# Kernel tuning notes

Measured on AMD Instinct MI355X. Metric: run time of the kernel, lower is better.

## Reference

```python
import jax, jax.numpy as jnp
import numpy as np

# Gemma3-style config (matches init_kwargs)
NUM_HEADS = 8
NUM_KV_GROUPS = 4
HEAD_DIM = 256
GROUP_SIZE = NUM_HEADS // NUM_KV_GROUPS
SLIDING_WINDOW = 1024
QUERY_PRE_ATTN_SCALAR = 256.0
SCALE = QUERY_PRE_ATTN_SCALAR ** (-0.5)
EPS = 1e-6


def rmsnorm(x, scale):
    # Gemma-style RMSNorm: fp32 variance, zero-centered weight with (1 + scale)
    xf = x.astype(jnp.float32)
    var = jnp.mean(xf * xf, axis=-1, keepdims=True)
    out = xf * jax.lax.rsqrt(var + EPS) * (1.0 + scale.astype(jnp.float32))
    return out.astype(x.dtype)


def sliding_causal_mask(q_len, kv_len, dtype):
    # additive mask [q_len, kv_len]: 0 allowed, -inf blocked
    q_pos = jnp.arange(kv_len - q_len, kv_len)[:, None]
    k_pos = jnp.arange(kv_len)[None, :]
    allowed = (k_pos <= q_pos) & (k_pos >= q_pos - SLIDING_WINDOW + 1)
    return jnp.where(allowed, jnp.zeros((), dtype), jnp.array(-jnp.inf, dtype))


def setup_inputs() -> dict:
    key = jax.random.key(0)
    ks = jax.random.split(key, 5)
    B, T, D = 2, 2048, 2560
    H, G, Hd = NUM_HEADS, NUM_KV_GROUPS, HEAD_DIM
    x = jax.random.normal(ks[0], (B, T, D), dtype=jnp.float32)
    Wq = jax.random.normal(ks[1], (D, H * Hd), dtype=jnp.float32) * 0.02
    Wk = jax.random.normal(ks[2], (D, G * Hd), dtype=jnp.float32) * 0.02
    Wv = jax.random.normal(ks[3], (D, G * Hd), dtype=jnp.float32) * 0.02
    Wo = jax.random.normal(ks[4], (H * Hd, D), dtype=jnp.float32) * 0.02
    q_scale = jnp.zeros((Hd,), dtype=jnp.float32)
    k_scale = jnp.zeros((Hd,), dtype=jnp.float32)
    return {"x": x, "Wq": Wq, "Wk": Wk, "Wv": Wv, "Wo": Wo,
            "q_scale": q_scale, "k_scale": k_scale}


def reference(x, Wq, Wk, Wv, Wo, q_scale, k_scale):
    B, T, D = x.shape
    H, G, g, Hd = NUM_HEADS, NUM_KV_GROUPS, GROUP_SIZE, HEAD_DIM
    # projections
    q = (x @ Wq).reshape(B, T, H, Hd).transpose(0, 2, 1, 3)   # [B,H,T,Hd]
    k = (x @ Wk).reshape(B, T, G, Hd).transpose(0, 2, 1, 3)   # [B,G,T,Hd]
    v = (x @ Wv).reshape(B, T, G, Hd).transpose(0, 2, 1, 3)   # [B,G,T,Hd]
    # qk-norm
    q = rmsnorm(q, q_scale)
    k = rmsnorm(k, k_scale)
    S = T  # no past_kv (prefill)
    # faithful reproduction of the module's head-group reshapes
    q = q.reshape(B, G, g, T, Hd).reshape(B * g, G, T, Hd)
    k = jnp.broadcast_to(k[:, None], (B, g, G, S, Hd)).reshape(B * g, G, S, Hd)
    v = jnp.broadcast_to(v[:, None], (B, g, G, S, Hd)).reshape(B * g, G, S, Hd)
    mask = sliding_causal_mask(T, S, q.dtype)  # [T,S]
    scores = jnp.einsum('bgtd,bgsd->bgts', q, k) * SCALE + mask
    attn = jax.nn.softmax(scores, axis=-1)
    out = jnp.einsum('bgts,bgsd->bgtd', attn, v)
    # faithful inverse reshapes (note g/G order swap vs input, as in source)
    out = out.reshape(B, g, G, T, Hd).reshape(B, H, T, Hd)
    out = out.transpose(0, 2, 1, 3).reshape(B, T, H * Hd)
    return out @ Wo
```

## Files before the change

### kernel.cpp

```cpp
#include <hip/hip_runtime.h>
#include <hip/hip_bf16.h>

typedef unsigned short u16;

#define T_SEQ 2048
#define NTOK 4096
#define D_MODEL 2560
#define NQKV 4096
#define WIN 1024
#define ATTN_SCALE 0.0625f
#define SMAX 17.0f
#define KROW 264

typedef __attribute__((ext_vector_type(8))) short bf16x8;
typedef __attribute__((ext_vector_type(8))) unsigned short u16x8;
typedef __attribute__((ext_vector_type(4))) float f32x4;

__device__ __forceinline__ float bf2f(u16 u) {
  union { unsigned int i; float f; } c; c.i = ((unsigned int)u) << 16; return c.f;
}
__device__ __forceinline__ u16 f2bf(float f) {
  __hip_bfloat16 h = __float2bfloat16(f);
  return __builtin_bit_cast(u16, h);
}
__device__ __forceinline__ u16x8 load8f(const float* p) {
  float4 a = *(const float4*)p;
  float4 b = *(const float4*)(p + 4);
  u16x8 r;
  r[0] = f2bf(a.x); r[1] = f2bf(a.y); r[2] = f2bf(a.z); r[3] = f2bf(a.w);
  r[4] = f2bf(b.x); r[5] = f2bf(b.y); r[6] = f2bf(b.z); r[7] = f2bf(b.w);
  return r;
}
__device__ __forceinline__ void gload_lds16(const u16* g, u16* l) {
  __builtin_amdgcn_global_load_lds(
      (const __attribute__((address_space(1))) void*)g,
      (__attribute__((address_space(3))) void*)l, 16, 0, 0);
}

__global__ __launch_bounds__(256) void cvt_f32_bf16(
    const float* __restrict__ in, u16* __restrict__ out) {
  size_t i = ((size_t)blockIdx.x * 256 + threadIdx.x) * 8;
  *(u16x8*)(out + i) = load8f(in + i);
}

__global__ __launch_bounds__(256) void transpose_w(
    const float* __restrict__ in, u16* __restrict__ out, int K, int N) {
  __shared__ u16 tile[64][65];
  int kb = blockIdx.y * 64, nb = blockIdx.x * 64;
  int t = threadIdx.x;
  int c4 = (t & 15) * 4;
  int r0 = t >> 4;
#pragma unroll
  for (int i = 0; i < 4; ++i) {
    int r = r0 + i * 16;
    float4 v = *(const float4*)(in + (size_t)(kb + r) * N + nb + c4);
    tile[r][c4] = f2bf(v.x); tile[r][c4 + 1] = f2bf(v.y);
    tile[r][c4 + 2] = f2bf(v.z); tile[r][c4 + 3] = f2bf(v.w);
  }
  __syncthreads();
#pragma unroll
  for (int i = 0; i < 4; ++i) {
    int n = r0 + i * 16;
    ushort4 v;
    v.x = tile[c4 + 0][n];
    v.y = tile[c4 + 1][n];
    v.z = tile[c4 + 2][n];
    v.w = tile[c4 + 3][n];
    *(ushort4*)(out + (size_t)(nb + n) * K + kb + c4) = v;
  }
}

__global__ __launch_bounds__(256) void v_transpose(
    const u16* __restrict__ qkv, u16* __restrict__ Vt) {
  int bg = blockIdx.z; int b = bg >> 2, g = bg & 3;
  __shared__ u16 tile[64][65];
  int tb = blockIdx.y * 64, db = blockIdx.x * 64;
  const u16* in = qkv + (size_t)(b * T_SEQ) * NQKV + 3072 + g * 256;
  u16* out = Vt + (size_t)bg * 256 * T_SEQ;
  int t = threadIdx.x;
  int c4 = (t & 15) * 4;
  int r0 = t >> 4;
#pragma unroll
  for (int i = 0; i < 4; ++i) {
    int r = r0 + i * 16;
    ushort4 v = *(const ushort4*)(in + (size_t)(tb + r) * NQKV + db + c4);
    tile[r][c4] = v.x; tile[r][c4 + 1] = v.y; tile[r][c4 + 2] = v.z; tile[r][c4 + 3] = v.w;
  }
  __syncthreads();
#pragma unroll
  for (int i = 0; i < 4; ++i) {
    int n = r0 + i * 16;
    ushort4 v;
    v.x = tile[c4 + 0][n];
    v.y = tile[c4 + 1][n];
    v.z = tile[c4 + 2][n];
    v.w = tile[c4 + 3][n];
    *(ushort4*)(out + (size_t)(db + n) * T_SEQ + tb + c4) = v;
  }
}

template <int WC>
__global__ __launch_bounds__(256, 2) void gemm_fast(
    const u16* __restrict__ A, int lda, const u16* __restrict__ Bt, int ldb,
    void* __restrict__ C, int ldc, int K) {
  __shared__ __align__(16) u16 As[128 * 32];
  __shared__ __align__(16) u16 Bs[128 * 32];
  const int tid = threadIdx.x;
  const int wave = tid >> 6, lane = tid & 63;
  const int quad = lane >> 4, l16 = lane & 15;
  const int mblk = blockIdx.y * 128, nblk = blockIdx.x * 128;
  const int wm = (wave >> 1) * 64, wn = (wave & 1) * 64;
  f32x4 acc[4][4] = {};
  const int c0 = wave * 2;
  for (int k0 = 0; k0 < K; k0 += 32) {
#pragma unroll
    for (int i = 0; i < 2; ++i) {
      int c = c0 + i;
      int flat = c * 64 + lane;
      int row = flat >> 2;
      int kb = (flat & 3) * 8;
      gload_lds16(A + (size_t)(mblk + row) * lda + k0 + kb, As + c * 512);
      gload_lds16(Bt + (size_t)(nblk + row) * ldb + k0 + kb, Bs + c * 512);
    }
    __syncthreads();
    bf16x8 aF[4], bF[4];
#pragma unroll
    for (int t = 0; t < 4; ++t) {
      aF[t] = *(const bf16x8*)(As + (wm + t * 16 + l16) * 32 + quad * 8);
      bF[t] = *(const bf16x8*)(Bs + (wn + t * 16 + l16) * 32 + quad * 8);
    }
#pragma unroll
    for (int tm = 0; tm < 4; ++tm)
#pragma unroll
      for (int tn = 0; tn < 4; ++tn)
        acc[tm][tn] = __builtin_amdgcn_mfma_f32_16x16x32_bf16(aF[tm], bF[tn], acc[tm][tn], 0, 0, 0);
    __syncthreads();
  }
#pragma unroll
  for (int tm = 0; tm < 4; ++tm)
#pragma unroll
    for (int tn = 0; tn < 4; ++tn)
#pragma unroll
      for (int r = 0; r < 4; ++r) {
        int row = mblk + wm + tm * 16 + quad * 4 + r;
        int col = nblk + wn + tn * 16 + l16;
        if constexpr (WC)
          ((float*)C)[(size_t)row * ldc + col] = acc[tm][tn][r];
        else
          ((u16*)C)[(size_t)row * ldc + col] = f2bf(acc[tm][tn][r]);
      }
}

__global__ __launch_bounds__(256, 2) void gemm_f32a(
    const float* __restrict__ A, int lda, const u16* __restrict__ Bt, int ldb,
    u16* __restrict__ C, int ldc, int K) {
  __shared__ __align__(16) u16 As[128 * 32];
  __shared__ __align__(16) u16 Bs[128 * 32];
  const int tid = threadIdx.x;
  const int wave = tid >> 6, lane = tid & 63;
  const int quad = lane >> 4, l16 = lane & 15;
  const int mblk = blockIdx.y * 128, nblk = blockIdx.x * 128;
  const int wm = (wave >> 1) * 64, wn = (wave & 1) * 64;
  f32x4 acc[4][4] = {};
  for (int k0 = 0; k0 < K; k0 += 32) {
#pragma unroll
    for (int i = 0; i < 2; ++i) {
      int u = i * 256 + tid;
      int row = u >> 2;
      int kb = (u & 3) * 8;
      *(u16x8*)(As + row * 32 + kb) = load8f(A + (size_t)(mblk + row) * lda + k0 + kb);
      *(u16x8*)(Bs + row * 32 + kb) = *(const u16x8*)(Bt + (size_t)(nblk + row) * ldb + k0 + kb);
    }
    __syncthreads();
    bf16x8 aF[4], bF[4];
#pragma unroll
    for (int t = 0; t < 4; ++t) {
      aF[t] = *(const bf16x8*)(As + (wm + t * 16 + l16) * 32 + quad * 8);
      bF[t] = *(const bf16x8*)(Bs + (wn + t * 16 + l16) * 32 + quad * 8);
    }
#pragma unroll
    for (int tm = 0; tm < 4; ++tm)
#pragma unroll
      for (int tn = 0; tn < 4; ++tn)
        acc[tm][tn] = __builtin_amdgcn_mfma_f32_16x16x32_bf16(aF[tm], bF[tn], acc[tm][tn], 0, 0, 0);
    __syncthreads();
  }
#pragma unroll
  for (int tm = 0; tm < 4; ++tm)
#pragma unroll
    for (int tn = 0; tn < 4; ++tn)
#pragma unroll
      for (int r = 0; r < 4; ++r) {
        int row = mblk + wm + tm * 16 + quad * 4 + r;
        int col = nblk + wn + tn * 16 + l16;
        C[(size_t)row * ldc + col] = f2bf(acc[tm][tn][r]);
      }
}

__global__ __launch_bounds__(256) void rmsnorm_qk(
    u16* __restrict__ qkv, const float* __restrict__ q_scale,
    const float* __restrict__ k_scale) {
  int wv = blockIdx.x * 4 + (threadIdx.x >> 6);
  int lane = threadIdx.x & 63;
  int token = wv / 12, j = wv - token * 12;
  const float* sc = (j < 8) ? q_scale : k_scale;
  int col = (j < 8) ? j * 256 : 2048 + (j - 8) * 256;
  u16* p = qkv + (size_t)token * NQKV + col;
  int d = lane * 4;
  ushort4 raw = *(const ushort4*)(p + d);
  float x0 = bf2f(raw.x), x1 = bf2f(raw.y), x2 = bf2f(raw.z), x3 = bf2f(raw.w);
  float sum = x0 * x0 + x1 * x1 + x2 * x2 + x3 * x3;
#pragma unroll
  for (int m = 1; m < 64; m <<= 1) sum += __shfl_xor(sum, m, 64);
  float r = rsqrtf(sum * (1.0f / 256.0f) + 1e-6f);
  float4 sv = *(const float4*)(sc + d);
  ushort4 o;
  o.x = f2bf(x0 * r * (1.0f + sv.x));
  o.y = f2bf(x1 * r * (1.0f + sv.y));
  o.z = f2bf(x2 * r * (1.0f + sv.z));
  o.w = f2bf(x3 * r * (1.0f + sv.w));
  *(ushort4*)(p + d) = o;
}

__global__ __launch_bounds__(256) void attn_fused(
    u16* __restrict__ qkv, const u16* __restrict__ Vt) {
  const int qt = blockIdx.x, h = blockIdx.y, b = blockIdx.z;
  const int g = h & 3;
  const int tid = threadIdx.x;
  const int wave = tid >> 6, lane = tid & 63;
  const int quad = lane >> 4, l16 = lane & 15;
  const int t0 = qt * 64;
  const int tw = t0 + wave * 16;
  __shared__ __align__(16) u16 Ks[32 * KROW];
  __shared__ __align__(16) u16 Vs[256 * 32];
  __shared__ __align__(16) u16 Ps[4][16 * 32];
  bf16x8 qF[8];
  {
    const u16* qrow = qkv + (size_t)(b * T_SEQ + tw + l16) * NQKV + h * 256;
#pragma unroll
    for (int kc = 0; kc < 8; ++kc)
      qF[kc] = *(const bf16x8*)(qrow + kc * 32 + quad * 8);
  }
  const u16* vt_base = Vt + (size_t)(b * 4 + g) * 256 * T_SEQ;
  f32x4 o[16] = {};
  float lsum[4] = {0.f, 0.f, 0.f, 0.f};
  int s_lo = t0 - (WIN - 1); if (s_lo < 0) s_lo = 0; s_lo &= ~31;
  const int s_hi = t0 + 63;
  for (int sb = s_lo; sb <= s_hi; sb += 32) {
#pragma unroll
    for (int i = 0; i < 4; ++i) {
      int u = i * 256 + tid;
      int krow = u >> 5, kcb = u & 31;
      *(u16x8*)(Ks + krow * KROW + kcb * 8) =
          *(const u16x8*)(qkv + (size_t)(b * T_SEQ + sb + krow) * NQKV + 2048 + g * 256 + kcb * 8);
      int dim = u >> 2, kvp = (u & 3) * 8;
      *(u16x8*)(Vs + dim * 32 + kvp) =
          *(const u16x8*)(vt_base + (size_t)dim * T_SEQ + sb + kvp);
    }
    __syncthreads();
    f32x4 st[2] = {};
#pragma unroll
    for (int nt = 0; nt < 2; ++nt)
#pragma unroll
      for (int kc = 0; kc < 8; ++kc) {
        bf16x8 kF = *(const bf16x8*)(Ks + (nt * 16 + l16) * KROW + kc * 32 + quad * 8);
        st[nt] = __builtin_amdgcn_mfma_f32_16x16x32_bf16(qF[kc], kF, st[nt], 0, 0, 0);
      }
    const bool full = (sb + 31 <= tw) && (sb >= tw + 15 - (WIN - 1));
#pragma unroll
    for (int r = 0; r < 4; ++r) {
      float v0 = st[0][r] * ATTN_SCALE - SMAX;
      float v1 = st[1][r] * ATTN_SCALE - SMAX;
      if (!full) {
        int t = tw + quad * 4 + r;
        int c0s = sb + l16, c1s = c0s + 16;
        v0 = (c0s <= t && c0s > t - WIN) ? v0 : -3.0e38f;
        v1 = (c1s <= t && c1s > t - WIN) ? v1 : -3.0e38f;
      }
      float p0 = __expf(v0);
      float p1 = __expf(v1);
      Ps[wave][(quad * 4 + r) * 32 + l16] = f2bf(p0);
      Ps[wave][(quad * 4 + r) * 32 + 16 + l16] = f2bf(p1);
      lsum[r] += p0 + p1;
    }
    __syncthreads();
    bf16x8 pF = *(const bf16x8*)(&Ps[wave][l16 * 32 + quad * 8]);
#pragma unroll
    for (int nt = 0; nt < 16; ++nt) {
      bf16x8 vF = *(const bf16x8*)(Vs + (nt * 16 + l16) * 32 + quad * 8);
      o[nt] = __builtin_amdgcn_mfma_f32_16x16x32_bf16(pF, vF, o[nt], 0, 0, 0);
    }
    __syncthreads();
  }
#pragma unroll
  for (int r = 0; r < 4; ++r) {
    float s = lsum[r];
    s += __shfl_xor(s, 1, 64);
    s += __shfl_xor(s, 2, 64);
    s += __shfl_xor(s, 4, 64);
    s += __shfl_xor(s, 8, 64);
    lsum[r] = s;
  }
#pragma unroll
  for (int r = 0; r < 4; ++r) {
    float inv = 1.0f / lsum[r];
    int t = tw + quad * 4 + r;
    u16* orow = qkv + (size_t)(b * T_SEQ + t) * NQKV + h * 256;
#pragma unroll
    for (int nt = 0; nt < 16; ++nt)
      orow[nt * 16 + l16] = f2bf(o[nt][r] * inv);
  }
}

extern "C" void kernel_launch(void* const* d_in, const int* in_sizes, int n_in,
                              void* d_out, int out_size, void* d_ws, size_t ws_size,
                              hipStream_t stream) {
  const float* x       = (const float*)d_in[0];
  const float* Wq      = (const float*)d_in[1];
  const float* Wk      = (const float*)d_in[2];
  const float* Wv      = (const float*)d_in[3];
  const float* Wo      = (const float*)d_in[4];
  const float* q_scale = (const float*)d_in[5];
  const float* k_scale = (const float*)d_in[6];

  u16* qkv = (u16*)d_ws;
  const size_t BIG_WS = (size_t)NTOK * NQKV * 2
                      + (size_t)NTOK * D_MODEL * 2
                      + (size_t)NQKV * D_MODEL * 2;

  if (ws_size >= BIG_WS) {
    u16* xbf = qkv + (size_t)NTOK * NQKV;
    u16* WT  = xbf + (size_t)NTOK * D_MODEL;
    cvt_f32_bf16<<<dim3(NTOK * D_MODEL / (256 * 8)), 256, 0, stream>>>(x, xbf);
    transpose_w<<<dim3(32, 40), 256, 0, stream>>>(Wq, WT, D_MODEL, 2048);
    transpose_w<<<dim3(16, 40), 256, 0, stream>>>(Wk, WT + (size_t)2048 * D_MODEL, D_MODEL, 1024);
    transpose_w<<<dim3(16, 40), 256, 0, stream>>>(Wv, WT + (size_t)3072 * D_MODEL, D_MODEL, 1024);
    gemm_fast<0><<<dim3(32, 32), 256, 0, stream>>>(xbf, D_MODEL, WT, D_MODEL, qkv, NQKV, D_MODEL);
    rmsnorm_qk<<<dim3(12288), 256, 0, stream>>>(qkv, q_scale, k_scale);
    v_transpose<<<dim3(4, 32, 8), 256, 0, stream>>>(qkv, xbf);
    attn_fused<<<dim3(T_SEQ / 64, 8, 2), 256, 0, stream>>>(qkv, xbf);
    transpose_w<<<dim3(40, 32), 256, 0, stream>>>(Wo, WT, 2048, D_MODEL);
    gemm_fast<1><<<dim3(20, 32), 256, 0, stream>>>(qkv, NQKV, WT, 2048, d_out, D_MODEL, 2048);
  } else {
    u16* WT = qkv + (size_t)NTOK * NQKV;
    transpose_w<<<dim3(32, 40), 256, 0, stream>>>(Wq, WT, D_MODEL, 2048);
    gemm_f32a<<<dim3(16, 32), 256, 0, stream>>>(x, D_MODEL, WT, D_MODEL, qkv, NQKV, D_MODEL);
    transpose_w<<<dim3(16, 40), 256, 0, stream>>>(Wk, WT, D_MODEL, 1024);
    gemm_f32a<<<dim3(8, 32), 256, 0, stream>>>(x, D_MODEL, WT, D_MODEL, qkv + 2048, NQKV, D_MODEL);
    transpose_w<<<dim3(16, 40), 256, 0, stream>>>(Wv, WT, D_MODEL, 1024);
    gemm_f32a<<<dim3(8, 32), 256, 0, stream>>>(x, D_MODEL, WT, D_MODEL, qkv + 3072, NQKV, D_MODEL);
    rmsnorm_qk<<<dim3(12288), 256, 0, stream>>>(qkv, q_scale, k_scale);
    v_transpose<<<dim3(4, 32, 8), 256, 0, stream>>>(qkv, WT);
    attn_fused<<<dim3(T_SEQ / 64, 8, 2), 256, 0, stream>>>(qkv, WT);
    transpose_w<<<dim3(40, 32), 256, 0, stream>>>(Wo, WT, 2048, D_MODEL);
    gemm_fast<1><<<dim3(20, 32), 256, 0, stream>>>(qkv, NQKV, WT, 2048, d_out, D_MODEL, 2048);
  }
}
```

Baseline: 406.2 us.

## Add 256x256-tile pipelined GEMM with async LDS loads for QKV and output projections

Adds a new GEMM kernel with 256x256 block tiles, 8 waves, and a 4-slot LDS ring filled by direct global-to-LDS loads with XOR swizzling. It issues three stages ahead and splits each k-step into two halves with barriers and s_setprio around the MFMA bursts. It also remaps block IDs to group neighbouring tiles. Both projection GEMMs on the large-workspace path switch to it, aiming for more data reuse and better load/compute overlap. The cost is 128KB of dynamic LDS per block and fewer blocks: 256 for QKV and 160 for the output projection, which can leave CUs idle.

```diff
diff --git a/kernel.cpp b/kernel.cpp
--- a/kernel.cpp
+++ b/kernel.cpp
@@ -97,6 +97,108 @@
     v.w = tile[c4 + 3][n];
     *(ushort4*)(out + (size_t)(db + n) * T_SEQ + tb + c4) = v;
   }
+}
+
+template <int WC>
+__global__ __launch_bounds__(512, 2) void gemm_256(
+    const u16* __restrict__ A, int lda, const u16* __restrict__ Bt, int ldb,
+    void* __restrict__ C, int ldc, int K) {
+  extern __shared__ ulong2 LDSraw[];
+  u16* SA = (u16*)LDSraw;
+  u16* SB = SA + 32768;
+  const int tid = threadIdx.x;
+  const int wave = tid >> 6, lane = tid & 63;
+  const int quad = lane >> 4, l16 = lane & 15;
+  const int gx = gridDim.x;
+  const int orig = blockIdx.y * gx + blockIdx.x;
+  const int cpx = (gx * gridDim.y) >> 3;
+  const int swz = (orig & 7) * cpx + (orig >> 3);
+  const int mblk = (swz / gx) * 256, nblk = (swz % gx) * 256;
+  const int wm = (wave >> 2) * 128, wn = (wave & 3) * 64;
+
+  const u16* srcA[2]; const u16* srcB[2];
+  int ldsOff[2];
+#pragma unroll
+  for (int i = 0; i < 2; ++i) {
+    int u = i * 512 + tid;
+    int hi3 = (u & 7) ^ ((u >> 3) & 7);
+    int r = ((u >> 3) << 1) | (hi3 >> 2);
+    int cbe = (hi3 & 3) << 3;
+    srcA[i] = A + (size_t)(mblk + r) * lda + cbe;
+    srcB[i] = Bt + (size_t)(nblk + r) * ldb + cbe;
+    ldsOff[i] = (u >> 6) << 9;
+  }
+  const int unit = ((((l16 & 1) << 2) | quad) ^ ((l16 >> 1) & 7)) << 3;
+  const int base_a = ((wm >> 1) + (l16 >> 1)) * 64 + unit;
+  const int base_b = ((wn >> 1) + (l16 >> 1)) * 64 + unit;
+  const int NK = K >> 5;
+  f32x4 acc[8][4] = {};
+
+  auto stage = [&](int s, int i) {
+    int slot = s & 3;
+    gload_lds16(srcA[i] + s * 32, SA + slot * 8192 + ldsOff[i]);
+    gload_lds16(srcB[i] + s * 32, SB + slot * 8192 + ldsOff[i]);
+  };
+
+  stage(0, 0); stage(0, 1); stage(1, 0); stage(1, 1); stage(2, 0); stage(2, 1);
+  asm volatile("s_waitcnt vmcnt(8)" ::: "memory");
+  __builtin_amdgcn_s_barrier();
+  asm volatile("" ::: "memory");
+
+  for (int s = 0; s < NK; ++s) {
+    const u16* sa = SA + (s & 3) * 8192;
+    const u16* sb = SB + (s & 3) * 8192;
+    bf16x8 aF[4], bF[4];
+#pragma unroll
+    for (int t = 0; t < 4; ++t) aF[t] = *(const bf16x8*)(sa + base_a + t * 512);
+#pragma unroll
+    for (int t = 0; t < 4; ++t) bF[t] = *(const bf16x8*)(sb + base_b + t * 512);
+    if (s + 3 < NK) stage(s + 3, 0);
+    asm volatile("" ::: "memory");
+    __builtin_amdgcn_s_barrier();
+    asm volatile("" ::: "memory");
+    __builtin_amdgcn_s_setprio(1);
+#pragma unroll
+    for (int m = 0; m < 4; ++m)
+#pragma unroll
+      for (int n = 0; n < 4; ++n)
+        acc[m][n] = __builtin_amdgcn_mfma_f32_16x16x32_bf16(aF[m], bF[n], acc[m][n], 0, 0, 0);
+    __builtin_amdgcn_s_setprio(0);
+    asm volatile("" ::: "memory");
+    __builtin_amdgcn_s_barrier();
+    asm volatile("" ::: "memory");
+#pragma unroll
+    for (int t = 0; t < 4; ++t) aF[t] = *(const bf16x8*)(sa + base_a + (t + 4) * 512);
+    if (s + 3 < NK) stage(s + 3, 1);
+    asm volatile("" ::: "memory");
+    __builtin_amdgcn_s_barrier();
+    asm volatile("" ::: "memory");
+    __builtin_amdgcn_s_setprio(1);
+#pragma unroll
+    for (int m = 0; m < 4; ++m)
+#pragma unroll
+      for (int n = 0; n < 4; ++n)
+        acc[m + 4][n] = __builtin_amdgcn_mfma_f32_16x16x32_bf16(aF[m], bF[n], acc[m + 4][n], 0, 0, 0);
+    __builtin_amdgcn_s_setprio(0);
+    if (s < NK - 3)       asm volatile("s_waitcnt vmcnt(8)" ::: "memory");
+    else if (s == NK - 3) asm volatile("s_waitcnt vmcnt(4)" ::: "memory");
+    else if (s == NK - 2) asm volatile("s_waitcnt vmcnt(0)" ::: "memory");
+    __builtin_amdgcn_s_barrier();
+    asm volatile("" ::: "memory");
+  }
+#pragma unroll
+  for (int m = 0; m < 8; ++m)
+#pragma unroll
+    for (int n = 0; n < 4; ++n)
+#pragma unroll
+      for (int r = 0; r < 4; ++r) {
+        int row = mblk + wm + m * 16 + quad * 4 + r;
+        int col = nblk + wn + n * 16 + l16;
+        if constexpr (WC)
+          ((float*)C)[(size_t)row * ldc + col] = acc[m][n][r];
+        else
+          ((u16*)C)[(size_t)row * ldc + col] = f2bf(acc[m][n][r]);
+      }
 }
 
 template <int WC>
@@ -329,18 +431,22 @@
                       + (size_t)NQKV * D_MODEL * 2;
 
   if (ws_size >= BIG_WS) {
+    (void)hipFuncSetAttribute(reinterpret_cast<const void*>(&gemm_256<0>),
+                              hipFuncAttributeMaxDynamicSharedMemorySize, 131072);
+    (void)hipFuncSetAttribute(reinterpret_cast<const void*>(&gemm_256<1>),
+                              hipFuncAttributeMaxDynamicSharedMemorySize, 131072);
     u16* xbf = qkv + (size_t)NTOK * NQKV;
     u16* WT  = xbf + (size_t)NTOK * D_MODEL;
     cvt_f32_bf16<<<dim3(NTOK * D_MODEL / (256 * 8)), 256, 0, stream>>>(x, xbf);
     transpose_w<<<dim3(32, 40), 256, 0, stream>>>(Wq, WT, D_MODEL, 2048);
     transpose_w<<<dim3(16, 40), 256, 0, stream>>>(Wk, WT + (size_t)2048 * D_MODEL, D_MODEL, 1024);
     transpose_w<<<dim3(16, 40), 256, 0, stream>>>(Wv, WT + (size_t)3072 * D_MODEL, D_MODEL, 1024);
-    gemm_fast<0><<<dim3(32, 32), 256, 0, stream>>>(xbf, D_MODEL, WT, D_MODEL, qkv, NQKV, D_MODEL);
+    gemm_256<0><<<dim3(16, 16), 512, 131072, stream>>>(xbf, D_MODEL, WT, D_MODEL, qkv, NQKV, D_MODEL);
     rmsnorm_qk<<<dim3(12288), 256, 0, stream>>>(qkv, q_scale, k_scale);
     v_transpose<<<dim3(4, 32, 8), 256, 0, stream>>>(qkv, xbf);
     attn_fused<<<dim3(T_SEQ / 64, 8, 2), 256, 0, stream>>>(qkv, xbf);
     transpose_w<<<dim3(40, 32), 256, 0, stream>>>(Wo, WT, 2048, D_MODEL);
-    gemm_fast<1><<<dim3(20, 32), 256, 0, stream>>>(qkv, NQKV, WT, 2048, d_out, D_MODEL, 2048);
+    gemm_256<1><<<dim3(10, 16), 512, 131072, stream>>>(qkv, NQKV, WT, 2048, d_out, D_MODEL, 2048);
   } else {
     u16* WT = qkv + (size_t)NTOK * NQKV;
     transpose_w<<<dim3(32, 40), 256, 0, stream>>>(Wq, WT, D_MODEL, 2048);
```

Measured after the change: 388.8 us. -4.3%, faster.
